# Kernel optimization log

Measured on AMD Instinct MI355X. Metric: run time of the kernel, lower is better.

The kernel has to match this reference:

```python
import jax, jax.numpy as jnp
import numpy as np

B, T, D = 4, 2048, 1024
H, HD = 16, 64  # n_heads, head_dim; H*HD == D

def setup_inputs() -> dict:
    key = jax.random.key(0)
    ks = jax.random.split(key, 9)
    s = 1.0 / np.sqrt(D)
    return {
        "x": jax.random.normal(ks[0], (B, T, D), dtype=jnp.float32),
        "Wq": jax.random.normal(ks[1], (D, D), dtype=jnp.float32) * s,
        "bq": jnp.zeros((D,), dtype=jnp.float32),
        "Wk": jax.random.normal(ks[2], (D, D), dtype=jnp.float32) * s,
        "bk": jnp.zeros((D,), dtype=jnp.float32),
        "Wv": jax.random.normal(ks[3], (D, D), dtype=jnp.float32) * s,
        "bv": jnp.zeros((D,), dtype=jnp.float32),
        "Wo": jax.random.normal(ks[4], (D, D), dtype=jnp.float32) * s,
        "bo": jnp.zeros((D,), dtype=jnp.float32),
    }

def reference(x, Wq, bq, Wk, bk, Wv, bv, Wo, bo):
    # Linear(in,out): y = x @ W.T + b (weights stored [out,in])
    q = (jnp.einsum('btd,ed->bte', x, Wq) + bq).reshape(B, T, H, HD).transpose(0, 2, 1, 3)
    k = (jnp.einsum('btd,ed->bte', x, Wk) + bk).reshape(B, T, H, HD).transpose(0, 2, 1, 3)
    v = (jnp.einsum('btd,ed->bte', x, Wv) + bv).reshape(B, T, H, HD).transpose(0, 2, 1, 3)
    scale = jnp.sqrt(jnp.asarray(HD, dtype=x.dtype))
    attn = jnp.einsum('bhqd,bhkd->bhqk', q, k) / scale  # [B,H,T,T]
    attn = jax.nn.softmax(attn, axis=-1)
    out = jnp.einsum('bhqk,bhkd->bhqd', attn, v)
    out = out.transpose(0, 2, 1, 3).reshape(B, T, H * HD)
    return jnp.einsum('bte,de->btd', out, Wo) + bo
```

## Files before the change

### kernel.cpp

```cpp
#include <hip/hip_runtime.h>
#include <hip/hip_bf16.h>

#define B_ 4
#define T_ 2048
#define D_ 1024
#define H_ 16
#define HD_ 64
#define M_ (B_ * T_)

typedef __attribute__((ext_vector_type(8))) short   s16x8;
typedef __attribute__((ext_vector_type(4))) short   s16x4;
typedef __attribute__((ext_vector_type(4))) float   f32x4;
typedef __attribute__((ext_vector_type(4))) float   fvec4;
typedef __attribute__((ext_vector_type(4))) unsigned short u16x4;

union U4 { u16x4 v; unsigned int w[2]; };
union P2 { s16x4 v; unsigned int w[2]; };

__device__ inline unsigned short f2bf(float f) {
    unsigned int u = __float_as_uint(f);
    return (unsigned short)((u + 0x7fffu + ((u >> 16) & 1u)) >> 16);
}

__device__ inline unsigned int pk_bf16(float a, float b) {
    unsigned int r;
    asm("v_cvt_pk_bf16_f32 %0, %1, %2" : "=v"(r) : "v"(a), "v"(b));
    return r;
}

__device__ inline f32x4 mfma32(s16x8 a, s16x8 b, f32x4 c) {
    return __builtin_amdgcn_mfma_f32_16x16x32_bf16(a, b, c, 0, 0, 0);
}

__device__ inline void gld16(const unsigned short* g, unsigned short* l) {
    __builtin_amdgcn_global_load_lds(
        (const __attribute__((address_space(1))) unsigned int*)g,
        (__attribute__((address_space(3))) unsigned int*)l, 16, 0, 0);
}

__global__ void cvt_all(const float* __restrict__ x,
                        const float* __restrict__ wq, const float* __restrict__ wk,
                        const float* __restrict__ wv, const float* __restrict__ wo,
                        unsigned short* __restrict__ xb, unsigned short* __restrict__ wcat) {
    const int bid = blockIdx.x;
    const float* src; unsigned short* dst; int off;
    if (bid < 8192)       { src = x;  dst = xb;                  off = bid; }
    else if (bid < 9216)  { src = wq; dst = wcat;                off = bid - 8192; }
    else if (bid < 10240) { src = wk; dst = wcat + 1 * 1048576;  off = bid - 9216; }
    else if (bid < 11264) { src = wv; dst = wcat + 2 * 1048576;  off = bid - 10240; }
    else                  { src = wo; dst = wcat + 3 * 1048576;  off = bid - 11264; }
    int i = off * 1024 + threadIdx.x * 4;
    fvec4 v = *(const fvec4*)(src + i);
    U4 o;
    o.w[0] = pk_bf16(v[0], v[1]);
    o.w[1] = pk_bf16(v[2], v[3]);
    *(u16x4*)(dst + i) = o.v;
}

#define GEMM_BODY(A_, W_)                                                          \
    __shared__ __align__(16) unsigned short As[2][128 * 32];                       \
    __shared__ __align__(16) unsigned short Bs[2][128 * 32];                       \
    const int tid = threadIdx.x;                                                   \
    const int wave = tid >> 6, lane = tid & 63;                                    \
    const int quad = lane >> 4, l16 = lane & 15;                                   \
    const int wr = (wave >> 1) * 64, wc = (wave & 1) * 64;                         \
    f32x4 acc[4][4] = {};                                                          \
    {                                                                              \
        for (int i = 0; i < 2; ++i) {                                              \
            int idx = tid + i * 256;                                               \
            int row = idx >> 2, c8 = (idx & 3) * 8;                                \
            gld16(A_ + (size_t)(m0 + row) * 1024 + c8, As[0] + idx * 8);           \
            gld16(W_ + (size_t)(n0 + row) * 1024 + c8, Bs[0] + idx * 8);           \
        }                                                                          \
    }                                                                              \
    for (int c = 0; c < 32; ++c) {                                                 \
        __syncthreads();                                                           \
        if (c + 1 < 32) {                                                          \
            int kn = (c + 1) * 32, nb = (c + 1) & 1;                               \
            for (int i = 0; i < 2; ++i) {                                          \
                int idx = tid + i * 256;                                           \
                int row = idx >> 2, c8 = (idx & 3) * 8;                            \
                gld16(A_ + (size_t)(m0 + row) * 1024 + kn + c8, As[nb] + idx * 8); \
                gld16(W_ + (size_t)(n0 + row) * 1024 + kn + c8, Bs[nb] + idx * 8); \
            }                                                                      \
        }                                                                          \
        const unsigned short* Ac = As[c & 1];                                      \
        const unsigned short* Bc = Bs[c & 1];                                      \
        s16x8 af[4], bfr[4];                                                       \
        for (int i = 0; i < 4; ++i)                                                \
            af[i] = *(const s16x8*)(Ac + (wr + i * 16 + l16) * 32 + quad * 8);     \
        for (int j = 0; j < 4; ++j)                                                \
            bfr[j] = *(const s16x8*)(Bc + (wc + j * 16 + l16) * 32 + quad * 8);    \
        for (int i = 0; i < 4; ++i)                                                \
            for (int j = 0; j < 4; ++j)                                            \
                acc[i][j] = mfma32(af[i], bfr[j], acc[i][j]);                      \
    }

__global__ __launch_bounds__(256) void gemm_qkv(
    const unsigned short* __restrict__ A, const unsigned short* __restrict__ Wcat,
    const float* __restrict__ bq, const float* __restrict__ bk, const float* __restrict__ bv,
    unsigned short* __restrict__ Qb, unsigned short* __restrict__ Kb,
    unsigned short* __restrict__ Vt, float qscale) {
    const int proj = blockIdx.y >> 3;
    const int m0 = blockIdx.x * 128, n0 = (blockIdx.y & 7) * 128;
    const unsigned short* W = Wcat + (size_t)proj * 1048576;
    const float* bias = proj == 0 ? bq : (proj == 1 ? bk : bv);

    GEMM_BODY(A, W)

    const float scale = (proj == 0) ? qscale : 1.0f;
    unsigned short* outp = (proj == 0) ? Qb : (proj == 1 ? Kb : Vt);
    for (int i = 0; i < 4; ++i) {
        int mbase = m0 + wr + i * 16 + quad * 4;
        int b = mbase >> 11, t = mbase & (T_ - 1);
        for (int j = 0; j < 4; ++j) {
            int n = n0 + wc + j * 16 + l16;
            float bi = bias[n];
            int h = n >> 6, hd = n & 63;
            if (proj == 2) {
                U4 o;
                o.w[0] = pk_bf16(acc[i][j][0] + bi, acc[i][j][1] + bi);
                o.w[1] = pk_bf16(acc[i][j][2] + bi, acc[i][j][3] + bi);
                *(u16x4*)(outp + ((size_t)(b * H_ + h) * HD_ + hd) * T_ + t) = o.v;
            } else {
                for (int r = 0; r < 4; ++r) {
                    float v = (acc[i][j][r] + bi) * scale;
                    outp[(((size_t)(b * H_ + h) * T_ + t + r) * HD_) + hd] = f2bf(v);
                }
            }
        }
    }
}

__global__ __launch_bounds__(256) void gemm_o(
    const unsigned short* __restrict__ A, const unsigned short* __restrict__ W,
    const float* __restrict__ bias, float* __restrict__ out) {
    const int m0 = blockIdx.x * 128, n0 = blockIdx.y * 128;

    GEMM_BODY(A, W)

    for (int i = 0; i < 4; ++i) {
        int mbase = m0 + wr + i * 16 + quad * 4;
        for (int j = 0; j < 4; ++j) {
            int n = n0 + wc + j * 16 + l16;
            float bi = bias[n];
            for (int r = 0; r < 4; ++r)
                out[(size_t)(mbase + r) * D_ + n] = acc[i][j][r] + bi;
        }
    }
}

__global__ __launch_bounds__(256) void attn(
    const unsigned short* __restrict__ Qb, const unsigned short* __restrict__ Kb,
    const unsigned short* __restrict__ Vt, unsigned short* __restrict__ Ob) {
    __shared__ __align__(16) unsigned short Ks[2 * 4096];
    __shared__ __align__(16) unsigned short Vs[2 * 4096];

    const int tid = threadIdx.x;
    const int wave = tid >> 6, lane = tid & 63;
    const int quad = lane >> 4, l16 = lane & 15;
    const int bh = blockIdx.y, b = bh >> 4, h = bh & 15;
    const int q0 = blockIdx.x * 128 + wave * 32;
    const unsigned short* Qp = Qb + (size_t)bh * T_ * HD_;
    const unsigned short* Kp = Kb + (size_t)bh * T_ * HD_;
    const unsigned short* Vp = Vt + (size_t)bh * HD_ * T_;

    s16x8 qf[2][2];
    for (int qt = 0; qt < 2; ++qt)
        for (int ds = 0; ds < 2; ++ds)
            qf[qt][ds] = *(const s16x8*)(Qp + (size_t)(q0 + qt * 16 + l16) * HD_ + ds * 32 + quad * 8);

    f32x4 accO[2][4] = {};
    float lst[2] = {0.f, 0.f};

    const int r0 = tid >> 3,           cg0 = (tid & 7) ^ (r0 & 7);
    const int r1 = (tid + 256) >> 3,   cg1 = (tid & 7) ^ (r1 & 7);

    const int xk  = quad ^ (l16 & 7);
    const int kro = l16 * 64 + xk * 8;
    const int kro1 = l16 * 64 + (xk ^ 4) * 8;

    auto stage = [&](int k0, int bufS) {
        gld16(Kp + (size_t)(k0 + r0) * HD_ + cg0 * 8, Ks + bufS + tid * 8);
        gld16(Kp + (size_t)(k0 + r1) * HD_ + cg1 * 8, Ks + bufS + (tid + 256) * 8);
        gld16(Vp + (size_t)r0 * T_ + k0 + cg0 * 8, Vs + bufS + tid * 8);
        gld16(Vp + (size_t)r1 * T_ + k0 + cg1 * 8, Vs + bufS + (tid + 256) * 8);
    };

    stage(0, 0);

    for (int c = 0; c < T_ / 64; ++c) {
        __syncthreads();

        if (c + 1 < T_ / 64) stage((c + 1) * 64, ((c + 1) & 1) * 4096);

        const unsigned short* Kc = Ks + (c & 1) * 4096;
        const unsigned short* Vc = Vs + (c & 1) * 4096;

        f32x4 st[2][4] = {};
        __builtin_amdgcn_s_setprio(1);
        for (int kt = 0; kt < 4; ++kt) {
            s16x8 kf0 = *(const s16x8*)(Kc + kt * 1024 + kro);
            s16x8 kf1 = *(const s16x8*)(Kc + kt * 1024 + kro1);
            for (int qt = 0; qt < 2; ++qt) {
                st[qt][kt] = mfma32(kf0, qf[qt][0], st[qt][kt]);
                st[qt][kt] = mfma32(kf1, qf[qt][1], st[qt][kt]);
            }
        }
        __builtin_amdgcn_s_setprio(0);

        s16x4 pb[2][4];
        for (int qt = 0; qt < 2; ++qt) {
            float rs = 0.f;
            for (int kt = 0; kt < 4; ++kt) {
                float p0 = __builtin_amdgcn_exp2f(st[qt][kt][0]);
                float p1 = __builtin_amdgcn_exp2f(st[qt][kt][1]);
                float p2 = __builtin_amdgcn_exp2f(st[qt][kt][2]);
                float p3 = __builtin_amdgcn_exp2f(st[qt][kt][3]);
                rs += (p0 + p1) + (p2 + p3);
                P2 pk;
                pk.w[0] = pk_bf16(p0, p1);
                pk.w[1] = pk_bf16(p2, p3);
                pb[qt][kt] = pk.v;
            }
            lst[qt] += rs;
        }

        __builtin_amdgcn_s_setprio(1);
        for (int u = 0; u < 2; ++u) {
            s16x8 pf0 = __builtin_shufflevector(pb[0][2 * u], pb[0][2 * u + 1],
                                                0, 1, 2, 3, 4, 5, 6, 7);
            s16x8 pf1 = __builtin_shufflevector(pb[1][2 * u], pb[1][2 * u + 1],
                                                0, 1, 2, 3, 4, 5, 6, 7);
            const int cA = 4 * u + (quad >> 1);
            for (int dt = 0; dt < 4; ++dt) {
                const unsigned short* vrow = Vc + (dt * 16 + l16) * 64 + (quad & 1) * 4;
                s16x4 vlo = *(const s16x4*)(vrow + ((cA       ^ (l16 & 7)) * 8));
                s16x4 vhi = *(const s16x4*)(vrow + (((cA + 2) ^ (l16 & 7)) * 8));
                s16x8 vf = __builtin_shufflevector(vlo, vhi, 0, 1, 2, 3, 4, 5, 6, 7);
                accO[0][dt] = mfma32(vf, pf0, accO[0][dt]);
                accO[1][dt] = mfma32(vf, pf1, accO[1][dt]);
            }
        }
        __builtin_amdgcn_s_setprio(0);
    }

    for (int qt = 0; qt < 2; ++qt) {
        float l = lst[qt];
        l += __shfl_xor(l, 16, 64);
        l += __shfl_xor(l, 32, 64);
        float inv = 1.f / l;
        int t = q0 + qt * 16 + l16;
        for (int dt = 0; dt < 4; ++dt) {
            U4 o;
            o.w[0] = pk_bf16(accO[qt][dt][0] * inv, accO[qt][dt][1] * inv);
            o.w[1] = pk_bf16(accO[qt][dt][2] * inv, accO[qt][dt][3] * inv);
            *(u16x4*)(Ob + ((size_t)b * T_ + t) * D_ + h * 64 + dt * 16 + quad * 4) = o.v;
        }
    }
}

extern "C" void kernel_launch(void* const* d_in, const int* in_sizes, int n_in,
                              void* d_out, int out_size, void* d_ws, size_t ws_size,
                              hipStream_t stream) {
    const float* x  = (const float*)d_in[0];
    const float* Wq = (const float*)d_in[1];
    const float* bq = (const float*)d_in[2];
    const float* Wk = (const float*)d_in[3];
    const float* bk = (const float*)d_in[4];
    const float* Wv = (const float*)d_in[5];
    const float* bv = (const float*)d_in[6];
    const float* Wo = (const float*)d_in[7];
    const float* bo = (const float*)d_in[8];
    float* out = (float*)d_out;

    const size_t SZ = (size_t)M_ * D_ * sizeof(unsigned short);
    unsigned short* xb   = (unsigned short*)d_ws;
    unsigned short* Qb   = (unsigned short*)((char*)d_ws + 1 * SZ);
    unsigned short* Kb   = (unsigned short*)((char*)d_ws + 2 * SZ);
    unsigned short* Vbt  = (unsigned short*)((char*)d_ws + 3 * SZ);
    unsigned short* Wcat = (unsigned short*)((char*)d_ws + 4 * SZ);
    unsigned short* Ob   = xb;

    const float qscale = 1.4426950408889634f / 8.0f;

    dim3 blk(256);
    cvt_all<<<dim3(12288), blk, 0, stream>>>(x, Wq, Wk, Wv, Wo, xb, Wcat);
    gemm_qkv<<<dim3(M_ / 128, 24), blk, 0, stream>>>(xb, Wcat, bq, bk, bv, Qb, Kb, Vbt, qscale);
    attn<<<dim3(T_ / 128, B_ * H_), blk, 0, stream>>>(Qb, Kb, Vbt, Ob);
    gemm_o<<<dim3(M_ / 128, D_ / 128), blk, 0, stream>>>(Ob, Wcat + 3 * 1048576, bo, out);
}
```

Before: 304.5 us.

## Swap MFMA operands for vectorized epilogues, MFMA row sums, and remap attention blocks

```diff
diff --git a/kernel.cpp b/kernel.cpp
--- a/kernel.cpp
+++ b/kernel.cpp
@@ -57,7 +57,7 @@
     *(u16x4*)(dst + i) = o.v;
 }
 
-#define GEMM_BODY(A_, W_)                                                          \
+#define GEMM_BODY(A_, W_, SWAPPED_)                                                \
     __shared__ __align__(16) unsigned short As[2][128 * 32];                       \
     __shared__ __align__(16) unsigned short Bs[2][128 * 32];                       \
     const int tid = threadIdx.x;                                                   \
@@ -91,9 +91,15 @@
             af[i] = *(const s16x8*)(Ac + (wr + i * 16 + l16) * 32 + quad * 8);     \
         for (int j = 0; j < 4; ++j)                                                \
             bfr[j] = *(const s16x8*)(Bc + (wc + j * 16 + l16) * 32 + quad * 8);    \
-        for (int i = 0; i < 4; ++i)                                                \
-            for (int j = 0; j < 4; ++j)                                            \
-                acc[i][j] = mfma32(af[i], bfr[j], acc[i][j]);                      \
+        if (SWAPPED_) {                                                            \
+            for (int i = 0; i < 4; ++i)                                            \
+                for (int j = 0; j < 4; ++j)                                        \
+                    acc[i][j] = mfma32(bfr[j], af[i], acc[i][j]);                  \
+        } else {                                                                   \
+            for (int i = 0; i < 4; ++i)                                            \
+                for (int j = 0; j < 4; ++j)                                        \
+                    acc[i][j] = mfma32(af[i], bfr[j], acc[i][j]);                  \
+        }                                                                          \
     }
 
 __global__ __launch_bounds__(256) void gemm_qkv(
@@ -105,28 +111,42 @@
     const int m0 = blockIdx.x * 128, n0 = (blockIdx.y & 7) * 128;
     const unsigned short* W = Wcat + (size_t)proj * 1048576;
     const float* bias = proj == 0 ? bq : (proj == 1 ? bk : bv);
-
-    GEMM_BODY(A, W)
-
-    const float scale = (proj == 0) ? qscale : 1.0f;
-    unsigned short* outp = (proj == 0) ? Qb : (proj == 1 ? Kb : Vt);
-    for (int i = 0; i < 4; ++i) {
-        int mbase = m0 + wr + i * 16 + quad * 4;
-        int b = mbase >> 11, t = mbase & (T_ - 1);
-        for (int j = 0; j < 4; ++j) {
-            int n = n0 + wc + j * 16 + l16;
-            float bi = bias[n];
-            int h = n >> 6, hd = n & 63;
-            if (proj == 2) {
+    const bool swapped = (proj != 2);
+
+    GEMM_BODY(A, W, swapped)
+
+    if (proj == 2) {
+        for (int i = 0; i < 4; ++i) {
+            int mbase = m0 + wr + i * 16 + quad * 4;
+            int b = mbase >> 11, t = mbase & (T_ - 1);
+            for (int j = 0; j < 4; ++j) {
+                int n = n0 + wc + j * 16 + l16;
+                float bi = bias[n];
+                int h = n >> 6, hd = n & 63;
                 U4 o;
                 o.w[0] = pk_bf16(acc[i][j][0] + bi, acc[i][j][1] + bi);
                 o.w[1] = pk_bf16(acc[i][j][2] + bi, acc[i][j][3] + bi);
-                *(u16x4*)(outp + ((size_t)(b * H_ + h) * HD_ + hd) * T_ + t) = o.v;
-            } else {
-                for (int r = 0; r < 4; ++r) {
-                    float v = (acc[i][j][r] + bi) * scale;
-                    outp[(((size_t)(b * H_ + h) * T_ + t + r) * HD_) + hd] = f2bf(v);
-                }
+                *(u16x4*)(Vt + ((size_t)(b * H_ + h) * HD_ + hd) * T_ + t) = o.v;
+            }
+        }
+    } else {
+        const float scale = (proj == 0) ? qscale : 1.0f;
+        unsigned short* outp = (proj == 0) ? Qb : Kb;
+        for (int i = 0; i < 4; ++i) {
+            int t = m0 + wr + i * 16 + l16;
+            int b = t >> 11, tt = t & (T_ - 1);
+            for (int j = 0; j < 4; ++j) {
+                int nb = n0 + wc + j * 16 + quad * 4;
+                fvec4 bi = *(const fvec4*)(bias + nb);
+                int h = nb >> 6, hd = nb & 63;
+                float v0 = (acc[i][j][0] + bi[0]) * scale;
+                float v1 = (acc[i][j][1] + bi[1]) * scale;
+                float v2 = (acc[i][j][2] + bi[2]) * scale;
+                float v3 = (acc[i][j][3] + bi[3]) * scale;
+                U4 o;
+                o.w[0] = pk_bf16(v0, v1);
+                o.w[1] = pk_bf16(v2, v3);
+                *(u16x4*)(outp + ((size_t)(b * H_ + h) * T_ + tt) * HD_ + hd) = o.v;
             }
         }
     }
@@ -137,15 +157,15 @@
     const float* __restrict__ bias, float* __restrict__ out) {
     const int m0 = blockIdx.x * 128, n0 = blockIdx.y * 128;
 
-    GEMM_BODY(A, W)
+    GEMM_BODY(A, W, true)
 
     for (int i = 0; i < 4; ++i) {
-        int mbase = m0 + wr + i * 16 + quad * 4;
+        int m = m0 + wr + i * 16 + l16;
         for (int j = 0; j < 4; ++j) {
-            int n = n0 + wc + j * 16 + l16;
-            float bi = bias[n];
-            for (int r = 0; r < 4; ++r)
-                out[(size_t)(mbase + r) * D_ + n] = acc[i][j][r] + bi;
+            int nb = n0 + wc + j * 16 + quad * 4;
+            fvec4 bi = *(const fvec4*)(bias + nb);
+            fvec4 o = acc[i][j] + bi;
+            *(fvec4*)(out + (size_t)m * D_ + nb) = o;
         }
     }
 }
@@ -159,8 +179,13 @@
     const int tid = threadIdx.x;
     const int wave = tid >> 6, lane = tid & 63;
     const int quad = lane >> 4, l16 = lane & 15;
-    const int bh = blockIdx.y, b = bh >> 4, h = bh & 15;
-    const int q0 = blockIdx.x * 128 + wave * 32;
+
+    const int flat = blockIdx.y * 16 + blockIdx.x;
+    const int wid  = (flat & 7) * 128 + (flat >> 3);
+    const int qblk = wid & 15, bh = wid >> 4;
+    const int b = bh >> 4, h = bh & 15;
+    const int q0 = qblk * 128 + wave * 32;
+
     const unsigned short* Qp = Qb + (size_t)bh * T_ * HD_;
     const unsigned short* Kp = Kb + (size_t)bh * T_ * HD_;
     const unsigned short* Vp = Vt + (size_t)bh * HD_ * T_;
@@ -171,7 +196,10 @@
             qf[qt][ds] = *(const s16x8*)(Qp + (size_t)(q0 + qt * 16 + l16) * HD_ + ds * 32 + quad * 8);
 
     f32x4 accO[2][4] = {};
-    float lst[2] = {0.f, 0.f};
+    f32x4 accL[2] = {};
+
+    const s16x8 ones = {0x3F80, 0x3F80, 0x3F80, 0x3F80,
+                        0x3F80, 0x3F80, 0x3F80, 0x3F80};
 
     const int r0 = tid >> 3,           cg0 = (tid & 7) ^ (r0 & 7);
     const int r1 = (tid + 256) >> 3,   cg1 = (tid & 7) ^ (r1 & 7);
@@ -211,19 +239,16 @@
 
         s16x4 pb[2][4];
         for (int qt = 0; qt < 2; ++qt) {
-            float rs = 0.f;
             for (int kt = 0; kt < 4; ++kt) {
                 float p0 = __builtin_amdgcn_exp2f(st[qt][kt][0]);
                 float p1 = __builtin_amdgcn_exp2f(st[qt][kt][1]);
                 float p2 = __builtin_amdgcn_exp2f(st[qt][kt][2]);
                 float p3 = __builtin_amdgcn_exp2f(st[qt][kt][3]);
-                rs += (p0 + p1) + (p2 + p3);
                 P2 pk;
                 pk.w[0] = pk_bf16(p0, p1);
                 pk.w[1] = pk_bf16(p2, p3);
                 pb[qt][kt] = pk.v;
             }
-            lst[qt] += rs;
         }
 
         __builtin_amdgcn_s_setprio(1);
@@ -232,6 +257,8 @@
                                                 0, 1, 2, 3, 4, 5, 6, 7);
             s16x8 pf1 = __builtin_shufflevector(pb[1][2 * u], pb[1][2 * u + 1],
                                                 0, 1, 2, 3, 4, 5, 6, 7);
+            accL[0] = mfma32(ones, pf0, accL[0]);
+            accL[1] = mfma32(ones, pf1, accL[1]);
             const int cA = 4 * u + (quad >> 1);
             for (int dt = 0; dt < 4; ++dt) {
                 const unsigned short* vrow = Vc + (dt * 16 + l16) * 64 + (quad & 1) * 4;
@@ -246,10 +273,7 @@
     }
 
     for (int qt = 0; qt < 2; ++qt) {
-        float l = lst[qt];
-        l += __shfl_xor(l, 16, 64);
-        l += __shfl_xor(l, 32, 64);
-        float inv = 1.f / l;
+        float inv = 1.f / accL[qt][0];
         int t = q0 + qt * 16 + l16;
         for (int dt = 0; dt < 4; ++dt) {
             U4 o;
```

Measured after the change: 316.2 us. 1.04x slower.
